# Optimization experiments

Measured on AMD Instinct MI355X. Metric: run time of the kernel, lower is better.

Reference implementation:

```python
import jax, jax.numpy as jnp
import numpy as np

EPS = 1e-6

def _aggregate(acc, right, a, w_acc, w_new):
    """Graded-logic weighted power mean aggregator.
    Andness a is mapped to a power-mean exponent r (a=0.5 -> r=1 arithmetic mean,
    a->1 -> r->-inf conjunctive, a->0 -> r->+inf disjunctive). Near r=0 the
    weighted geometric mean is the correct limit.
    """
    a_c = jnp.clip(a, EPS, 1.0 - EPS)
    r = (1.0 - 2.0 * a_c) / (a_c * (1.0 - a_c))
    use_geo = jnp.abs(r) < 1e-3
    r_safe = jnp.where(use_geo, 1.0, r)  # avoid inf in untaken branch
    acc_c = jnp.clip(acc, EPS, 1.0)
    right_c = jnp.clip(right, EPS, 1.0)
    pm = (w_acc * acc_c ** r_safe + w_new * right_c ** r_safe) ** (1.0 / r_safe)
    geo = acc_c ** w_acc * right_c ** w_new
    return jnp.where(use_geo, geo, pm)


def _forward(x, a_raw, w_raw):
    # andness mapping: sigmoid(a_raw) * 3 - 1  (normalize_andness=True)
    a_vec = jax.nn.sigmoid(a_raw) * 3.0 - 1.0
    # weight mapping: trainable + minmax normalization
    w_min, w_max = jnp.min(w_raw), jnp.max(w_raw)
    denom = jnp.maximum(w_max - w_min, 1e-8)
    w_new = jnp.clip((w_raw - w_min) / denom, 0.0, 1.0)
    w_acc = 1.0 - w_new

    leaf = x  # frozen identity permutation (is_frozen=True path)
    # first step (no NaN replacement in original)
    acc = _aggregate(leaf[:, 0], leaf[:, 1], a_vec[0], w_acc[0], w_new[0])

    def step(carry, inp):
        right, a_i, wa_i, wn_i = inp
        z = _aggregate(carry, right, a_i, wa_i, wn_i)
        z = jnp.where(jnp.isnan(z), a_i, z)  # per-step NaN patching
        return z, None

    xs = (leaf[:, 2:].T, a_vec[1:], w_acc[1:], w_new[1:])  # (L-1, B), (L-1,)...
    acc, _ = jax.lax.scan(step, acc, xs)
    return acc[:, None]  # (B, 1)


def setup_inputs() -> dict:
    key = jax.random.key(0)
    k1, k2 = jax.random.split(key)
    B, N = 524288, 64
    L = N - 1
    x = jax.random.uniform(k1, (B, N), dtype=jnp.float32)
    a_raw = jnp.zeros((L,), dtype=jnp.float32)
    w_raw = jax.random.uniform(k2, (L,), dtype=jnp.float32)
    return {"x": x, "a_raw": a_raw, "w_raw": w_raw}


def reference(x, a_raw, w_raw):
    return _forward(x, a_raw, w_raw)
```

## Files before the change

kernel.cpp:

```cpp
#include <hip/hip_runtime.h>

#define EPS 1e-6f
#define NSTEP 63

__device__ __forceinline__ float flog2(float x) { return __builtin_amdgcn_logf(x); }
__device__ __forceinline__ float fexp2(float x) { return __builtin_amdgcn_exp2f(x); }

__global__ __launch_bounds__(256, 2)
void vln_kernel(const float* __restrict__ x,
                const float* __restrict__ a_raw,
                const float* __restrict__ w_raw,
                float* __restrict__ out, int B) {
    __shared__ float4 tile[4][1024];
    __shared__ float s_wn[64];
    __shared__ float s_av[64];
    __shared__ float s_r[64];
    __shared__ int   s_geo[64];
    __shared__ int   s_allgeo;

    const int tid = threadIdx.x;

    if (tid < 64) {
        const int li = (tid < NSTEP) ? tid : 0;
        float w = w_raw[li];
        float wmin = w, wmax = w;
        #pragma unroll
        for (int off = 32; off > 0; off >>= 1) {
            wmin = fminf(wmin, __shfl_down(wmin, off));
            wmax = fmaxf(wmax, __shfl_down(wmax, off));
        }
        wmin = __shfl(wmin, 0);
        wmax = __shfl(wmax, 0);
        const float denom = fmaxf(wmax - wmin, 1e-8f);
        float wn = fminf(fmaxf((w - wmin) / denom, 0.0f), 1.0f);
        float ea = fexp2(-a_raw[li] * 1.4426950408889634f);
        float av = 3.0f / (1.0f + ea) - 1.0f;
        float ac = fminf(fmaxf(av, EPS), 1.0f - EPS);
        float r  = (1.0f - 2.0f * ac) / (ac * (1.0f - ac));
        int geo  = (fabsf(r) < 0.001f) ? 1 : 0;
        s_wn[tid] = wn;
        s_av[tid] = av;
        s_r[tid]  = r;
        s_geo[tid] = geo;
        unsigned long long m = __ballot(geo != 0 || tid >= NSTEP);
        if (tid == 0) s_allgeo = (m == ~0ULL) ? 1 : 0;
    }
    __syncthreads();

    const int wave = tid >> 6;
    const int lane = tid & 63;
    const long long rowbase = (long long)blockIdx.x * 256 + wave * 64;
    const long long row = rowbase + lane;

    float4 f[16];

    if (rowbase + 64 <= (long long)B) {
        const float4* g = (const float4*)(x + (size_t)rowbase * 64);
        float4* tl = tile[wave];
        #pragma unroll
        for (int t = 0; t < 16; ++t) {
            float4 v = g[t * 64 + lane];
            const int r  = t * 4 + (lane >> 4);
            const int gi = lane & 15;
            tl[r * 16 + (gi ^ (r & 15))] = v;
        }
        #pragma unroll
        for (int q = 0; q < 16; ++q)
            f[q] = tl[lane * 16 + (q ^ (lane & 15))];
    } else if (row < (long long)B) {
        const float4* xr = (const float4*)(x + (size_t)row * 64);
        #pragma unroll
        for (int q = 0; q < 16; ++q) f[q] = xr[q];
    }

    if (row >= (long long)B) return;

    if (s_allgeo) {
        float Lacc = 0.0f;
        #pragma unroll
        for (int q = 0; q < 16; ++q) {
            float el[4];
            el[0] = flog2(fminf(fmaxf(f[q].x, EPS), 1.0f));
            el[1] = flog2(fminf(fmaxf(f[q].y, EPS), 1.0f));
            el[2] = flog2(fminf(fmaxf(f[q].z, EPS), 1.0f));
            el[3] = flog2(fminf(fmaxf(f[q].w, EPS), 1.0f));
            #pragma unroll
            for (int j = 0; j < 4; ++j) {
                const int gidx = 4 * q + j;
                if (gidx == 0) { Lacc = el[0]; continue; }
                const float wn = s_wn[gidx - 1];
                Lacc = fmaf(wn, el[j] - Lacc, Lacc);
            }
        }
        out[row] = fexp2(Lacc);
    } else {
        float Lacc = 0.0f;
        float lin  = 0.0f;
        int use_lin = 0;
        #pragma unroll
        for (int q = 0; q < 16; ++q) {
            float el[4];
            el[0] = flog2(fminf(fmaxf(f[q].x, EPS), 1.0f));
            el[1] = flog2(fminf(fmaxf(f[q].y, EPS), 1.0f));
            el[2] = flog2(fminf(fmaxf(f[q].z, EPS), 1.0f));
            el[3] = flog2(fminf(fmaxf(f[q].w, EPS), 1.0f));
            #pragma unroll
            for (int j = 0; j < 4; ++j) {
                const int gidx = 4 * q + j;
                if (gidx == 0) { Lacc = el[0]; continue; }
                const int i = gidx - 1;
                const float wn = s_wn[i];
                const float lr = el[j];
                if (s_geo[i]) {
                    Lacc = fmaf(wn, lr - Lacc, Lacc);
                    use_lin = 0;
                } else {
                    const float r  = s_r[i];
                    const float pa = fexp2(r * Lacc);
                    const float pb = fexp2(r * lr);
                    const float s  = (1.0f - wn) * pa + wn * pb;
                    float z = fexp2(flog2(s) / r);
                    if (i > 0 && (z != z)) z = s_av[i];
                    lin = z; use_lin = 1;
                    Lacc = flog2(fminf(fmaxf(z, EPS), 1.0f));
                }
            }
        }
        out[row] = use_lin ? lin : fexp2(Lacc);
    }
}

extern "C" void kernel_launch(void* const* d_in, const int* in_sizes, int n_in,
                              void* d_out, int out_size, void* d_ws, size_t ws_size,
                              hipStream_t stream) {
    const float* x     = (const float*)d_in[0];
    const float* a_raw = (const float*)d_in[1];
    const float* w_raw = (const float*)d_in[2];
    float* out = (float*)d_out;
    const int B = out_size;
    const int blocks = (B + 255) / 256;
    vln_kernel<<<blocks, 256, 0, stream>>>(x, a_raw, w_raw, out, B);
}
```

Measured before the change: 193.1 us.

## Unroll geometric recurrence into weighted log-sum with coalesced 16-lane row reduction

Precomputes per-column coefficients (products of (1-w) suffixes times w) so the all-geometric chain becomes an independent weighted sum of log2 values. Each row is then handled by 16 lanes reading consecutive float4s and combined with xor-shuffle reductions, replacing the LDS transpose tile. A capped grid-stride loop with two loads in flight per iteration is used, and the clamp becomes a single med3. This removes the serial dependency chain and the shared-memory staging, at the cost of different float rounding from reassociating the recurrence.

```diff
diff --git a/kernel.cpp b/kernel.cpp
--- a/kernel.cpp
+++ b/kernel.cpp
@@ -5,13 +5,14 @@
 
 __device__ __forceinline__ float flog2(float x) { return __builtin_amdgcn_logf(x); }
 __device__ __forceinline__ float fexp2(float x) { return __builtin_amdgcn_exp2f(x); }
+__device__ __forceinline__ float clampe1(float x) { return __builtin_amdgcn_fmed3f(x, EPS, 1.0f); }
 
-__global__ __launch_bounds__(256, 2)
+__global__ __launch_bounds__(256, 8)
 void vln_kernel(const float* __restrict__ x,
                 const float* __restrict__ a_raw,
                 const float* __restrict__ w_raw,
-                float* __restrict__ out, int B) {
-    __shared__ float4 tile[4][1024];
+                float* __restrict__ out, long long B) {
+    __shared__ float s_c[64];
     __shared__ float s_wn[64];
     __shared__ float s_av[64];
     __shared__ float s_r[64];
@@ -44,89 +45,94 @@
         s_geo[tid] = geo;
         unsigned long long m = __ballot(geo != 0 || tid >= NSTEP);
         if (tid == 0) s_allgeo = (m == ~0ULL) ? 1 : 0;
+
+        float S = (tid < NSTEP) ? (1.0f - wn) : 1.0f;
+        #pragma unroll
+        for (int off = 1; off < 64; off <<= 1) {
+            float o = __shfl_down(S, off);
+            if (tid + off < 64) S *= o;
+        }
+        float wprev = __shfl_up(wn, 1);
+        s_c[tid] = (tid == 0) ? S : wprev * S;
     }
     __syncthreads();
 
-    const int wave = tid >> 6;
-    const int lane = tid & 63;
-    const long long rowbase = (long long)blockIdx.x * 256 + wave * 64;
-    const long long row = rowbase + lane;
-
-    float4 f[16];
-
-    if (rowbase + 64 <= (long long)B) {
-        const float4* g = (const float4*)(x + (size_t)rowbase * 64);
-        float4* tl = tile[wave];
-        #pragma unroll
-        for (int t = 0; t < 16; ++t) {
-            float4 v = g[t * 64 + lane];
-            const int r  = t * 4 + (lane >> 4);
-            const int gi = lane & 15;
-            tl[r * 16 + (gi ^ (r & 15))] = v;
-        }
-        #pragma unroll
-        for (int q = 0; q < 16; ++q)
-            f[q] = tl[lane * 16 + (q ^ (lane & 15))];
-    } else if (row < (long long)B) {
-        const float4* xr = (const float4*)(x + (size_t)row * 64);
-        #pragma unroll
-        for (int q = 0; q < 16; ++q) f[q] = xr[q];
-    }
-
-    if (row >= (long long)B) return;
+    const long long total4 = B * 16;
+    const long long stride = (long long)gridDim.x * blockDim.x;
+    long long idx0 = (long long)blockIdx.x * blockDim.x + tid;
 
     if (s_allgeo) {
-        float Lacc = 0.0f;
-        #pragma unroll
-        for (int q = 0; q < 16; ++q) {
-            float el[4];
-            el[0] = flog2(fminf(fmaxf(f[q].x, EPS), 1.0f));
-            el[1] = flog2(fminf(fmaxf(f[q].y, EPS), 1.0f));
-            el[2] = flog2(fminf(fmaxf(f[q].z, EPS), 1.0f));
-            el[3] = flog2(fminf(fmaxf(f[q].w, EPS), 1.0f));
+        const int k = tid & 15;
+        const float c0 = s_c[4 * k + 0];
+        const float c1 = s_c[4 * k + 1];
+        const float c2 = s_c[4 * k + 2];
+        const float c3 = s_c[4 * k + 3];
+        const float4* __restrict__ x4 = (const float4*)x;
+
+        for (long long i = idx0; i < total4; i += 2 * stride) {
+            const long long i1 = i + stride;
+            const bool has1 = (i1 < total4);
+            float4 v0 = x4[i];
+            float4 v1 = has1 ? x4[i1] : make_float4(1.f, 1.f, 1.f, 1.f);
+
+            float p0 = c0 * flog2(clampe1(v0.x));
+            p0 = fmaf(c1, flog2(clampe1(v0.y)), p0);
+            p0 = fmaf(c2, flog2(clampe1(v0.z)), p0);
+            p0 = fmaf(c3, flog2(clampe1(v0.w)), p0);
+            p0 += __shfl_xor(p0, 1);
+            p0 += __shfl_xor(p0, 2);
+            p0 += __shfl_xor(p0, 4);
+            p0 += __shfl_xor(p0, 8);
+            if (k == 0) out[i >> 4] = fexp2(p0);
+
+            float p1 = c0 * flog2(clampe1(v1.x));
+            p1 = fmaf(c1, flog2(clampe1(v1.y)), p1);
+            p1 = fmaf(c2, flog2(clampe1(v1.z)), p1);
+            p1 = fmaf(c3, flog2(clampe1(v1.w)), p1);
+            p1 += __shfl_xor(p1, 1);
+            p1 += __shfl_xor(p1, 2);
+            p1 += __shfl_xor(p1, 4);
+            p1 += __shfl_xor(p1, 8);
+            if (has1 && k == 0) out[i1 >> 4] = fexp2(p1);
+        }
+    } else {
+        for (long long row = idx0; row < B; row += stride) {
+            const float4* xr = (const float4*)(x + (size_t)row * 64);
+            float Lacc = 0.0f;
+            float lin  = 0.0f;
+            int use_lin = 0;
             #pragma unroll
-            for (int j = 0; j < 4; ++j) {
-                const int gidx = 4 * q + j;
-                if (gidx == 0) { Lacc = el[0]; continue; }
-                const float wn = s_wn[gidx - 1];
-                Lacc = fmaf(wn, el[j] - Lacc, Lacc);
-            }
-        }
-        out[row] = fexp2(Lacc);
-    } else {
-        float Lacc = 0.0f;
-        float lin  = 0.0f;
-        int use_lin = 0;
-        #pragma unroll
-        for (int q = 0; q < 16; ++q) {
-            float el[4];
-            el[0] = flog2(fminf(fmaxf(f[q].x, EPS), 1.0f));
-            el[1] = flog2(fminf(fmaxf(f[q].y, EPS), 1.0f));
-            el[2] = flog2(fminf(fmaxf(f[q].z, EPS), 1.0f));
-            el[3] = flog2(fminf(fmaxf(f[q].w, EPS), 1.0f));
-            #pragma unroll
-            for (int j = 0; j < 4; ++j) {
-                const int gidx = 4 * q + j;
-                if (gidx == 0) { Lacc = el[0]; continue; }
-                const int i = gidx - 1;
-                const float wn = s_wn[i];
-                const float lr = el[j];
-                if (s_geo[i]) {
-                    Lacc = fmaf(wn, lr - Lacc, Lacc);
-                    use_lin = 0;
-                } else {
-                    const float r  = s_r[i];
-                    const float pa = fexp2(r * Lacc);
-                    const float pb = fexp2(r * lr);
-                    const float s  = (1.0f - wn) * pa + wn * pb;
-                    float z = fexp2(flog2(s) / r);
-                    if (i > 0 && (z != z)) z = s_av[i];
-                    lin = z; use_lin = 1;
-                    Lacc = flog2(fminf(fmaxf(z, EPS), 1.0f));
+            for (int q = 0; q < 16; ++q) {
+                float4 v = xr[q];
+                float el[4];
+                el[0] = flog2(clampe1(v.x));
+                el[1] = flog2(clampe1(v.y));
+                el[2] = flog2(clampe1(v.z));
+                el[3] = flog2(clampe1(v.w));
+                #pragma unroll
+                for (int j = 0; j < 4; ++j) {
+                    const int gidx = 4 * q + j;
+                    if (gidx == 0) { Lacc = el[0]; continue; }
+                    const int i = gidx - 1;
+                    const float wn = s_wn[i];
+                    const float lr = el[j];
+                    if (s_geo[i]) {
+                        Lacc = fmaf(wn, lr - Lacc, Lacc);
+                        use_lin = 0;
+                    } else {
+                        const float r  = s_r[i];
+                        const float pa = fexp2(r * Lacc);
+                        const float pb = fexp2(r * lr);
+                        const float s  = (1.0f - wn) * pa + wn * pb;
+                        float z = fexp2(flog2(s) / r);
+                        if (i > 0 && (z != z)) z = s_av[i];
+                        lin = z; use_lin = 1;
+                        Lacc = flog2(clampe1(z));
+                    }
                 }
             }
+            out[row] = use_lin ? lin : fexp2(Lacc);
         }
-        out[row] = use_lin ? lin : fexp2(Lacc);
     }
 }
 
@@ -137,7 +143,9 @@
     const float* a_raw = (const float*)d_in[1];
     const float* w_raw = (const float*)d_in[2];
     float* out = (float*)d_out;
-    const int B = out_size;
-    const int blocks = (B + 255) / 256;
+    const long long B = out_size;
+    long long total4 = B * 16;
+    int blocks = (int)((total4 + 255) / 256);
+    if (blocks > 2048) blocks = 2048;
     vln_kernel<<<blocks, 256, 0, stream>>>(x, a_raw, w_raw, out, B);
 }
```

After: 191.6 us. No clear change (-0.8%).
